# Kernel optimization log

Measured on AMD Instinct MI355X. Metric: run time of the kernel, lower is better.

## Reference

```python
import jax, jax.numpy as jnp
import numpy as np

TEMPERATURE = 0.07
EPS = 1e-12  # matches torch F.normalize default eps


def setup_inputs() -> dict:
    key = jax.random.key(0)
    k1, k2 = jax.random.split(key)
    B, D = 8192, 256
    anchor = jax.random.normal(k1, (B, D), dtype=jnp.float32)
    positive = jax.random.normal(k2, (B, D), dtype=jnp.float32)
    return {"anchor": anchor, "positive": positive}


def _l2_normalize(x):
    # torch F.normalize(p=2, dim=1): x / max(||x||, eps)
    n = jnp.sqrt(jnp.sum(x * x, axis=1, keepdims=True))
    return x / jnp.maximum(n, EPS)


def reference(anchor, positive):
    a = _l2_normalize(anchor)
    p = _l2_normalize(positive)
    # normalized vectors -> cosine similarity is just a GEMM: (B, B)
    sim = jnp.einsum('id,jd->ij', a, p)
    B = sim.shape[0]
    # hard negative mining: max over off-diagonal entries per row
    neg = jnp.where(jnp.eye(B, dtype=bool), -jnp.inf, sim)
    max_neg = jnp.max(neg, axis=-1)  # (B,)
    logits = jnp.concatenate([sim, max_neg[:, None]], axis=1) / TEMPERATURE  # (B, B+1)
    labels = jnp.arange(B)
    logp = jax.nn.log_softmax(logits, axis=-1)
    loss = -jnp.mean(jnp.take_along_axis(logp, labels[:, None], axis=1))
    return loss
```

## Files before the change

kernel.cpp:

```cpp
#include <hip/hip_runtime.h>
#include <hip/hip_bf16.h>

using floatx4 = __attribute__((ext_vector_type(4))) float;
using int4v   = __attribute__((ext_vector_type(4))) int;
using int8v   = __attribute__((ext_vector_type(8))) int;

#define TEMP_INV 14.285714285714286f
#define DD 256
#define BM 128
#define BROWS 64
#define NCT 8
#define SC1 127

__global__ __launch_bounds__(256) void nrm_kernel(
    const float* __restrict__ anchor, const float* __restrict__ positive,
    unsigned char* __restrict__ a8, unsigned char* __restrict__ p8,
    float* __restrict__ diag, float* __restrict__ out) {
  if (blockIdx.x == 0 && threadIdx.x == 0) out[0] = 0.f;
  const int t = threadIdx.x;
  const int s = t & 15;
  const int r = t >> 4;
  const int row = blockIdx.x * 16 + r;
  const float4* av = (const float4*)(anchor   + (size_t)row * DD + s * 16);
  const float4* pv = (const float4*)(positive + (size_t)row * DD + s * 16);
  float4 va[4], vp[4];
  float sa = 0.f, sp = 0.f;
#pragma unroll
  for (int k = 0; k < 4; ++k) {
    va[k] = av[k]; vp[k] = pv[k];
    sa += va[k].x * va[k].x + va[k].y * va[k].y + va[k].z * va[k].z + va[k].w * va[k].w;
    sp += vp[k].x * vp[k].x + vp[k].y * vp[k].y + vp[k].z * vp[k].z + vp[k].w * vp[k].w;
  }
#pragma unroll
  for (int m = 1; m < 16; m <<= 1) {
    sa += __shfl_xor(sa, m, 16);
    sp += __shfl_xor(sp, m, 16);
  }
  const float ka = 1.0f / fmaxf(sqrtf(sa), 1e-12f);
  const float kp = 1.0f / fmaxf(sqrtf(sp), 1e-12f);
  int pa[4], pq[4];
#pragma unroll
  for (int k = 0; k < 4; ++k) {
    int x = __builtin_amdgcn_cvt_pk_fp8_f32(va[k].x * ka, va[k].y * ka, 0, false);
    pa[k] = __builtin_amdgcn_cvt_pk_fp8_f32(va[k].z * ka, va[k].w * ka, x, true);
    int y = __builtin_amdgcn_cvt_pk_fp8_f32(vp[k].x * kp, vp[k].y * kp, 0, false);
    pq[k] = __builtin_amdgcn_cvt_pk_fp8_f32(vp[k].z * kp, vp[k].w * kp, y, true);
  }
  *(int4v*)(a8 + (size_t)row * DD + s * 16) = (int4v){pa[0], pa[1], pa[2], pa[3]};
  {
    const unsigned int off = (unsigned)blockIdx.x * 4096 + ((s >> 3) << 11)
                           + ((s & 1) << 10) + (((s >> 1) & 3) << 8) + (r << 4);
    *(int4v*)(p8 + off) = (int4v){pq[0], pq[1], pq[2], pq[3]};
  }
  float d = 0.f;
#pragma unroll
  for (int k = 0; k < 4; ++k) {
    d += __builtin_amdgcn_cvt_f32_fp8(pa[k], 0) * __builtin_amdgcn_cvt_f32_fp8(pq[k], 0)
       + __builtin_amdgcn_cvt_f32_fp8(pa[k], 1) * __builtin_amdgcn_cvt_f32_fp8(pq[k], 1)
       + __builtin_amdgcn_cvt_f32_fp8(pa[k], 2) * __builtin_amdgcn_cvt_f32_fp8(pq[k], 2)
       + __builtin_amdgcn_cvt_f32_fp8(pa[k], 3) * __builtin_amdgcn_cvt_f32_fp8(pq[k], 3);
  }
#pragma unroll
  for (int m = 1; m < 16; m <<= 1) d += __shfl_xor(d, m, 16);
  if (s == 0) diag[row] = d;
}

__device__ __forceinline__ int8v fragG(const unsigned char* g) {
  const int4v lo = *(const int4v*)(g);
  const int4v hi = *(const int4v*)(g + 16);
  return __builtin_shufflevector(lo, hi, 0, 1, 2, 3, 4, 5, 6, 7);
}

__device__ __forceinline__ floatx4 mfma_sc(int8v a, int8v b, floatx4 c) {
  return __builtin_amdgcn_mfma_scale_f32_16x16x128_f8f6f4(a, b, c, 0, 0, 0,
                                                          SC1, 0, SC1);
}

__global__ __launch_bounds__(512, 4) void gemm_stats(
    const unsigned char* __restrict__ a8, const unsigned char* __restrict__ p8,
    float* __restrict__ rsum, float* __restrict__ rmax, int Btot) {
  __shared__ float red_sum[4][BROWS];
  __shared__ float red_max[4][BROWS];

  const int t = threadIdx.x;
  const int wave = t >> 6, lane = t & 63;
  const int wm = wave & 1, wn = wave >> 1;
  const int quad = lane >> 4, l16 = lane & 15;
  const int row0    = blockIdx.y * BROWS;
  const int colbase = blockIdx.x * (NCT * BM);
  const bool hasdiag = ((int)(blockIdx.y >> 4) == (int)blockIdx.x);

  int8v a_frag[2][2];
  {
    const unsigned char* ab =
        a8 + (size_t)(row0 + wm * 32 + l16) * DD + quad * 32;
#pragma unroll
    for (int mi = 0; mi < 2; ++mi)
#pragma unroll
      for (int ks = 0; ks < 2; ++ks)
        a_frag[mi][ks] = fragG(ab + mi * 16 * DD + ks * 128);
  }

  float se_run[2][4], mx_run[2][4];
#pragma unroll
  for (int a = 0; a < 2; ++a)
#pragma unroll
    for (int b = 0; b < 4; ++b) { se_run[a][b] = 0.f; mx_run[a][b] = -INFINITY; }

  for (int ct = 0; ct < NCT; ++ct) {
    const int col0 = colbase + ct * BM;
    const unsigned char* bb = p8 + (size_t)(col0 + wn * 32) * DD + lane * 16;

    floatx4 acc[2][2];
#pragma unroll
    for (int a = 0; a < 2; ++a)
#pragma unroll
      for (int b = 0; b < 2; ++b) acc[a][b] = (floatx4){0.f, 0.f, 0.f, 0.f};

#pragma unroll
    for (int ks = 0; ks < 2; ++ks) {
#pragma unroll
      for (int ni = 0; ni < 2; ++ni) {
        const unsigned char* c = bb + ni * 4096 + ks * 2048;
        const int4v lo = *(const int4v*)(c);
        const int4v hi = *(const int4v*)(c + 1024);
        const int8v bf = __builtin_shufflevector(lo, hi, 0, 1, 2, 3, 4, 5, 6, 7);
        acc[0][ni] = mfma_sc(a_frag[0][ks], bf, acc[0][ni]);
        acc[1][ni] = mfma_sc(a_frag[1][ks], bf, acc[1][ni]);
      }
    }

    if (!hasdiag) {
#pragma unroll
      for (int mi = 0; mi < 2; ++mi)
#pragma unroll
        for (int reg = 0; reg < 4; ++reg)
#pragma unroll
          for (int ni = 0; ni < 2; ++ni) {
            const float s = acc[mi][ni][reg];
            se_run[mi][reg] += __expf(s * TEMP_INV);
            mx_run[mi][reg] = fmaxf(mx_run[mi][reg], s);
          }
    } else {
#pragma unroll
      for (int mi = 0; mi < 2; ++mi)
#pragma unroll
        for (int reg = 0; reg < 4; ++reg) {
          const int i = row0 + wm * 32 + mi * 16 + quad * 4 + reg;
#pragma unroll
          for (int ni = 0; ni < 2; ++ni) {
            const float s = acc[mi][ni][reg];
            const int j = col0 + wn * 32 + ni * 16 + l16;
            se_run[mi][reg] += __expf(s * TEMP_INV);
            mx_run[mi][reg] = fmaxf(mx_run[mi][reg], (i == j) ? -INFINITY : s);
          }
        }
    }
  }

#pragma unroll
  for (int mi = 0; mi < 2; ++mi) {
#pragma unroll
    for (int reg = 0; reg < 4; ++reg) {
      float se = se_run[mi][reg], mx = mx_run[mi][reg];
#pragma unroll
      for (int m = 1; m < 16; m <<= 1) {
        se += __shfl_xor(se, m, 64);
        mx = fmaxf(mx, __shfl_xor(mx, m, 64));
      }
      if (l16 == 0) {
        const int rb = wm * 32 + mi * 16 + quad * 4 + reg;
        red_sum[wn][rb] = se;
        red_max[wn][rb] = mx;
      }
    }
  }
  __syncthreads();
  if (t < BROWS) {
    rsum[(size_t)blockIdx.x * Btot + row0 + t] =
        (red_sum[0][t] + red_sum[1][t]) + (red_sum[2][t] + red_sum[3][t]);
    rmax[(size_t)blockIdx.x * Btot + row0 + t] =
        fmaxf(fmaxf(red_max[0][t], red_max[1][t]),
              fmaxf(red_max[2][t], red_max[3][t]));
  }
}

__global__ __launch_bounds__(256) void row_loss_kernel(
    const float* __restrict__ rsum, const float* __restrict__ rmax,
    const float* __restrict__ diag, float* __restrict__ out, int Btot, int NG) {
  const int i = blockIdx.x * 256 + threadIdx.x;
  float s = 0.f, m = -INFINITY;
  for (int c = 0; c < NG; ++c) {
    s += rsum[(size_t)c * Btot + i];
    m = fmaxf(m, rmax[(size_t)c * Btot + i]);
  }
  float rl = __logf(s + __expf(m * TEMP_INV)) - diag[i] * TEMP_INV;
#pragma unroll
  for (int mm = 32; mm >= 1; mm >>= 1) rl += __shfl_xor(rl, mm, 64);
  __shared__ float red[4];
  if ((threadIdx.x & 63) == 0) red[threadIdx.x >> 6] = rl;
  __syncthreads();
  if (threadIdx.x == 0)
    atomicAdd(out, (red[0] + red[1] + red[2] + red[3]) / (float)Btot);
}

extern "C" void kernel_launch(void* const* d_in, const int* in_sizes, int n_in,
                              void* d_out, int out_size, void* d_ws, size_t ws_size,
                              hipStream_t stream) {
  const float* anchor   = (const float*)d_in[0];
  const float* positive = (const float*)d_in[1];
  const int B  = in_sizes[0] / DD;
  const int NG = B / (BM * NCT);
  const size_t BD = (size_t)B * DD;

  unsigned char* a8 = (unsigned char*)d_ws;
  unsigned char* p8 = a8 + BD;
  float* rsum  = (float*)(p8 + BD);
  float* rmax  = rsum + (size_t)NG * B;
  float* diag  = rmax + (size_t)NG * B;

  nrm_kernel<<<B / 16, 256, 0, stream>>>(anchor, positive, a8, p8, diag,
                                         (float*)d_out);
  dim3 g2(NG, B / BROWS);
  gemm_stats<<<g2, 512, 0, stream>>>(a8, p8, rsum, rmax, B);
  row_loss_kernel<<<B / 256, 256, 0, stream>>>(rsum, rmax, diag, (float*)d_out, B, NG);
}
```

Before: 102.7 us.

## Halve gemm block to 4 waves and double-buffer B fragment loads

The stats GEMM block shrinks from 8 waves to 4, so each block covers 64 columns per tile over 16 tiles instead of 128 columns over 8. The loop is unrolled by two with register double-buffering, so the next tile's B fragments are loaded while the current tile's MFMAs and exp/max reductions run. The aim is to hide global-load latency and raise per-wave work. In exchange, register pressure rises and there are fewer waves per block to hide latency, and the diagonal-tile check now depends on the tile index within the block.

```diff
diff --git a/kernel.cpp b/kernel.cpp
--- a/kernel.cpp
+++ b/kernel.cpp
@@ -7,9 +7,9 @@
 
 #define TEMP_INV 14.285714285714286f
 #define DD 256
-#define BM 128
 #define BROWS 64
-#define NCT 8
+#define BNC 64
+#define NCT 16
 #define SC1 127
 
 __global__ __launch_bounds__(256) void nrm_kernel(
@@ -76,19 +76,67 @@
                                                           SC1, 0, SC1);
 }
 
-__global__ __launch_bounds__(512, 4) void gemm_stats(
+#define LOADF(ct, buf)                                                        \
+  {                                                                           \
+    const unsigned char* bb_ = bbase + (size_t)(ct) * (BNC * DD);             \
+    _Pragma("unroll") for (int ks_ = 0; ks_ < 2; ++ks_)                       \
+    _Pragma("unroll") for (int ni_ = 0; ni_ < 2; ++ni_) {                     \
+      const unsigned char* c_ = bb_ + ni_ * 4096 + ks_ * 2048;                \
+      const int4v lo_ = *(const int4v*)(c_);                                  \
+      const int4v hi_ = *(const int4v*)(c_ + 1024);                           \
+      buf[ks_][ni_] =                                                         \
+          __builtin_shufflevector(lo_, hi_, 0, 1, 2, 3, 4, 5, 6, 7);          \
+    }                                                                         \
+  }
+
+#define COMPUTE(ct, buf)                                                      \
+  {                                                                           \
+    floatx4 acc[2][2];                                                        \
+    _Pragma("unroll") for (int a_ = 0; a_ < 2; ++a_)                          \
+    _Pragma("unroll") for (int b_ = 0; b_ < 2; ++b_)                          \
+        acc[a_][b_] = (floatx4){0.f, 0.f, 0.f, 0.f};                          \
+    _Pragma("unroll") for (int ks_ = 0; ks_ < 2; ++ks_)                       \
+    _Pragma("unroll") for (int ni_ = 0; ni_ < 2; ++ni_) {                     \
+      acc[0][ni_] = mfma_sc(a_frag[0][ks_], buf[ks_][ni_], acc[0][ni_]);      \
+      acc[1][ni_] = mfma_sc(a_frag[1][ks_], buf[ks_][ni_], acc[1][ni_]);      \
+    }                                                                         \
+    const int col0_ = colbase + (ct) * BNC;                                   \
+    const bool hd_ = hdbase && ((int)(blockIdx.y & 15) == (ct));              \
+    if (!hd_) {                                                               \
+      _Pragma("unroll") for (int mi_ = 0; mi_ < 2; ++mi_)                     \
+      _Pragma("unroll") for (int rg_ = 0; rg_ < 4; ++rg_)                     \
+      _Pragma("unroll") for (int ni_ = 0; ni_ < 2; ++ni_) {                   \
+        const float s_ = acc[mi_][ni_][rg_];                                  \
+        se_run[mi_][rg_] += __expf(s_ * TEMP_INV);                            \
+        mx_run[mi_][rg_] = fmaxf(mx_run[mi_][rg_], s_);                       \
+      }                                                                       \
+    } else {                                                                  \
+      _Pragma("unroll") for (int mi_ = 0; mi_ < 2; ++mi_)                     \
+      _Pragma("unroll") for (int rg_ = 0; rg_ < 4; ++rg_) {                   \
+        const int i_ = row0 + wm * 32 + mi_ * 16 + quad * 4 + rg_;            \
+        _Pragma("unroll") for (int ni_ = 0; ni_ < 2; ++ni_) {                 \
+          const float s_ = acc[mi_][ni_][rg_];                                \
+          const int j_ = col0_ + wn * 32 + ni_ * 16 + l16;                    \
+          se_run[mi_][rg_] += __expf(s_ * TEMP_INV);                          \
+          mx_run[mi_][rg_] = fmaxf(mx_run[mi_][rg_], (i_ == j_) ? -INFINITY : s_); \
+        }                                                                     \
+      }                                                                       \
+    }                                                                         \
+  }
+
+__global__ __launch_bounds__(256, 4) void gemm_stats(
     const unsigned char* __restrict__ a8, const unsigned char* __restrict__ p8,
     float* __restrict__ rsum, float* __restrict__ rmax, int Btot) {
-  __shared__ float red_sum[4][BROWS];
-  __shared__ float red_max[4][BROWS];
+  __shared__ float red_sum[2][BROWS];
+  __shared__ float red_max[2][BROWS];
 
   const int t = threadIdx.x;
   const int wave = t >> 6, lane = t & 63;
   const int wm = wave & 1, wn = wave >> 1;
   const int quad = lane >> 4, l16 = lane & 15;
   const int row0    = blockIdx.y * BROWS;
-  const int colbase = blockIdx.x * (NCT * BM);
-  const bool hasdiag = ((int)(blockIdx.y >> 4) == (int)blockIdx.x);
+  const int colbase = blockIdx.x * (NCT * BNC);
+  const bool hdbase = ((int)(blockIdx.y >> 4) == (int)blockIdx.x);
 
   int8v a_frag[2][2];
   {
@@ -101,61 +149,23 @@
         a_frag[mi][ks] = fragG(ab + mi * 16 * DD + ks * 128);
   }
 
+  const unsigned char* bbase =
+      p8 + (size_t)(colbase + wn * 32) * DD + lane * 16;
+
   float se_run[2][4], mx_run[2][4];
 #pragma unroll
   for (int a = 0; a < 2; ++a)
 #pragma unroll
     for (int b = 0; b < 4; ++b) { se_run[a][b] = 0.f; mx_run[a][b] = -INFINITY; }
 
-  for (int ct = 0; ct < NCT; ++ct) {
-    const int col0 = colbase + ct * BM;
-    const unsigned char* bb = p8 + (size_t)(col0 + wn * 32) * DD + lane * 16;
-
-    floatx4 acc[2][2];
-#pragma unroll
-    for (int a = 0; a < 2; ++a)
-#pragma unroll
-      for (int b = 0; b < 2; ++b) acc[a][b] = (floatx4){0.f, 0.f, 0.f, 0.f};
-
-#pragma unroll
-    for (int ks = 0; ks < 2; ++ks) {
-#pragma unroll
-      for (int ni = 0; ni < 2; ++ni) {
-        const unsigned char* c = bb + ni * 4096 + ks * 2048;
-        const int4v lo = *(const int4v*)(c);
-        const int4v hi = *(const int4v*)(c + 1024);
-        const int8v bf = __builtin_shufflevector(lo, hi, 0, 1, 2, 3, 4, 5, 6, 7);
-        acc[0][ni] = mfma_sc(a_frag[0][ks], bf, acc[0][ni]);
-        acc[1][ni] = mfma_sc(a_frag[1][ks], bf, acc[1][ni]);
-      }
-    }
-
-    if (!hasdiag) {
-#pragma unroll
-      for (int mi = 0; mi < 2; ++mi)
-#pragma unroll
-        for (int reg = 0; reg < 4; ++reg)
-#pragma unroll
-          for (int ni = 0; ni < 2; ++ni) {
-            const float s = acc[mi][ni][reg];
-            se_run[mi][reg] += __expf(s * TEMP_INV);
-            mx_run[mi][reg] = fmaxf(mx_run[mi][reg], s);
-          }
-    } else {
-#pragma unroll
-      for (int mi = 0; mi < 2; ++mi)
-#pragma unroll
-        for (int reg = 0; reg < 4; ++reg) {
-          const int i = row0 + wm * 32 + mi * 16 + quad * 4 + reg;
-#pragma unroll
-          for (int ni = 0; ni < 2; ++ni) {
-            const float s = acc[mi][ni][reg];
-            const int j = col0 + wn * 32 + ni * 16 + l16;
-            se_run[mi][reg] += __expf(s * TEMP_INV);
-            mx_run[mi][reg] = fmaxf(mx_run[mi][reg], (i == j) ? -INFINITY : s);
-          }
-        }
-    }
+  int8v b0[2][2], b1[2][2];
+  LOADF(0, b0);
+  for (int ct2 = 0; ct2 < NCT / 2; ++ct2) {
+    const int cta = 2 * ct2, ctb = 2 * ct2 + 1;
+    LOADF(ctb, b1);
+    COMPUTE(cta, b0);
+    if (ctb + 1 < NCT) LOADF(ctb + 1, b0);
+    COMPUTE(ctb, b1);
   }
 
 #pragma unroll
@@ -177,11 +187,9 @@
   }
   __syncthreads();
   if (t < BROWS) {
-    rsum[(size_t)blockIdx.x * Btot + row0 + t] =
-        (red_sum[0][t] + red_sum[1][t]) + (red_sum[2][t] + red_sum[3][t]);
+    rsum[(size_t)blockIdx.x * Btot + row0 + t] = red_sum[0][t] + red_sum[1][t];
     rmax[(size_t)blockIdx.x * Btot + row0 + t] =
-        fmaxf(fmaxf(red_max[0][t], red_max[1][t]),
-              fmaxf(red_max[2][t], red_max[3][t]));
+        fmaxf(red_max[0][t], red_max[1][t]);
   }
 }
 
@@ -210,7 +218,7 @@
   const float* anchor   = (const float*)d_in[0];
   const float* positive = (const float*)d_in[1];
   const int B  = in_sizes[0] / DD;
-  const int NG = B / (BM * NCT);
+  const int NG = B / (BNC * NCT);
   const size_t BD = (size_t)B * DD;
 
   unsigned char* a8 = (unsigned char*)d_ws;
@@ -222,6 +230,6 @@
   nrm_kernel<<<B / 16, 256, 0, stream>>>(anchor, positive, a8, p8, diag,
                                          (float*)d_out);
   dim3 g2(NG, B / BROWS);
-  gemm_stats<<<g2, 512, 0, stream>>>(a8, p8, rsum, rmax, B);
+  gemm_stats<<<g2, 256, 0, stream>>>(a8, p8, rsum, rmax, B);
   row_loss_kernel<<<B / 256, 256, 0, stream>>>(rsum, rmax, diag, (float*)d_out, B, NG);
 }
```

Measured after the change: 112.7 us. 9.7% more time.
